# Optimization experiments

Hardware: AMD Instinct MI355X
Metric: run time of the kernel (lower is better)

The kernel has to match this reference:

```python
import jax, jax.numpy as jnp
import numpy as np

D_MODEL = 1024
NHEAD = 16
HEAD_DIM = D_MODEL // NHEAD
LN_EPS = 1e-5


def _retention_scan(v, lam_h):
    # v: (B, L, H, DH); lam_h: (H,)
    # recurrence: s_0 = v_0; s_t = lam * s_{t-1} + v_t
    B, L, H, DH = v.shape
    a = jnp.broadcast_to(lam_h[None, None, :, None], v.shape)

    def combine(x, y):
        a1, b1 = x
        a2, b2 = y
        return (a1 * a2, a2 * b1 + b2)

    _, states = jax.lax.associative_scan(combine, (a, v), axis=1)
    return states


def setup_inputs() -> dict:
    key = jax.random.key(0)
    ks = jax.random.split(key, 6)
    B, L, D = 4, 4096, D_MODEL
    s = 1.0 / np.sqrt(D)
    return {
        "x": jax.random.normal(ks[0], (B, L, D), jnp.float32),
        "Wq": jax.random.normal(ks[1], (D, D), jnp.float32) * s,
        "Wv": jax.random.normal(ks[2], (D, D), jnp.float32) * s,
        "Wg": jax.random.normal(ks[3], (D, D), jnp.float32) * s,
        "Wo": jax.random.normal(ks[4], (D, D), jnp.float32) * s,
        "beta": jnp.full((NHEAD,), -0.2, jnp.float32),
        "ln_gamma": jnp.ones((D_MODEL,), jnp.float32),
        "ln_beta": jnp.zeros((D_MODEL,), jnp.float32),
    }


def reference(x, Wq, Wv, Wg, Wo, beta, ln_gamma, ln_beta):
    B, L, D = x.shape
    H, DH = NHEAD, HEAD_DIM
    # projections (torch Linear: x @ W.T)
    q = (x @ Wq.T).reshape(B, L, H, DH)
    v = (x @ Wv.T).reshape(B, L, H, DH)
    lam_h = jax.nn.sigmoid(beta)
    state = _retention_scan(v, lam_h)  # (B, L, H, DH)
    y = (q * state).reshape(B, L, D)
    # LayerNorm over last dim
    mu = jnp.mean(y, axis=-1, keepdims=True)
    var = jnp.mean((y - mu) ** 2, axis=-1, keepdims=True)
    y = (y - mu) * jax.lax.rsqrt(var + LN_EPS) * ln_gamma + ln_beta
    # SiLU gate
    gate = jax.nn.silu(x @ Wg.T)
    y = y * gate
    return y @ Wo.T
```

## Files before the change

kernel.cpp:

```cpp
#include <hip/hip_runtime.h>

#define BB 4
#define LL 4096
#define DM 1024
#define NH 16
#define MM (BB * LL)
#define CC2 256
#define LC2 16

typedef unsigned short u16;
typedef float f32x4 __attribute__((ext_vector_type(4)));
typedef __bf16 mfma_in __attribute__((ext_vector_type(8)));

__device__ __forceinline__ u16 f2bf(float f) {
    unsigned u = __float_as_uint(f);
    u += 0x7FFFu + ((u >> 16) & 1u);
    return (u16)(u >> 16);
}
__device__ __forceinline__ float bf2f(u16 u) {
    return __uint_as_float(((unsigned)u) << 16);
}

__device__ __forceinline__ void gld_lds16(const u16* g, u16* l) {
    __builtin_amdgcn_global_load_lds(
        (const __attribute__((address_space(1))) void*)g,
        (__attribute__((address_space(3))) void*)l,
        16, 0, 0);
}

#define XF4 (MM * DM / 4)
#define WF4 (DM * DM / 4)
__global__ __launch_bounds__(256)
void cvt_all(const float* __restrict__ x,
             const float* __restrict__ w0, const float* __restrict__ w1,
             const float* __restrict__ w2, const float* __restrict__ w3,
             u16* __restrict__ dst) {
    int i = blockIdx.x * 256 + threadIdx.x;
    const float* src;
    int si;
    if (i < XF4) { src = x; si = i; }
    else {
        int j = i - XF4;
        const float* ws[4] = {w0, w1, w2, w3};
        src = ws[j >> 18];
        si = j & (WF4 - 1);
    }
    float4 f = ((const float4*)src)[si];
    ushort4 o;
    o.x = f2bf(f.x); o.y = f2bf(f.y); o.z = f2bf(f.z); o.w = f2bf(f.w);
    ((ushort4*)dst)[i] = o;
}

__device__ __forceinline__ void mainloop_bk64(
    const u16* __restrict__ A, const u16* __restrict__ B, int K,
    int mBlk, int nBlk, u16* As, u16* Bs, f32x4 acc[4][4]) {
    const int tid  = threadIdx.x;
    const int wave = tid >> 6;
    const int lane = tid & 63;
    const int quad = lane >> 4;
    const int l16  = lane & 15;
    const int wm   = (wave >> 1) * 64;
    const int wn   = (wave & 1) * 64;

    const int srow8 = wave * 8 + (lane >> 3);
    const int cOff  = ((lane & 7) ^ (lane >> 3)) * 8;

    const u16* gA[4];
    const u16* gB[4];
    u16* lA[4];
    u16* lB[4];
#pragma unroll
    for (int j = 0; j < 4; j++) {
        gA[j] = A + (size_t)(mBlk + j * 32 + srow8) * K + cOff;
        gB[j] = B + (size_t)(nBlk + j * 32 + srow8) * K + cOff;
        lA[j] = As + (j * 32 + wave * 8) * 64;
        lB[j] = Bs + (j * 32 + wave * 8) * 64;
    }

    int rowA[4], rowB[4];
#pragma unroll
    for (int i = 0; i < 4; i++) {
        rowA[i] = (wm + i * 16 + l16) * 64;
        rowB[i] = (wn + i * 16 + l16) * 64;
    }
    const int c0 = ((quad    ) ^ (l16 & 7)) * 8;
    const int c1 = ((quad + 4) ^ (l16 & 7)) * 8;

    for (int kt = 0; kt < K; kt += 64) {
        __syncthreads();
#pragma unroll
        for (int j = 0; j < 4; j++) gld_lds16(gA[j] + kt, lA[j]);
#pragma unroll
        for (int j = 0; j < 4; j++) gld_lds16(gB[j] + kt, lB[j]);
        __syncthreads();

#pragma unroll
        for (int s = 0; s < 2; s++) {
            const int cs = s ? c1 : c0;
            mfma_in af[4], bfr[4];
#pragma unroll
            for (int i = 0; i < 4; i++)
                af[i] = *(const mfma_in*)&As[rowA[i] + cs];
#pragma unroll
            for (int j = 0; j < 4; j++)
                bfr[j] = *(const mfma_in*)&Bs[rowB[j] + cs];
#pragma unroll
            for (int i = 0; i < 4; i++)
#pragma unroll
                for (int j = 0; j < 4; j++)
                    acc[i][j] = __builtin_amdgcn_mfma_f32_16x16x32_bf16(af[i], bfr[j], acc[i][j], 0, 0, 0);
        }
    }
}

__global__ __launch_bounds__(256)
void gemm_qvg(const u16* __restrict__ A, const u16* __restrict__ B,
              u16* __restrict__ oq, u16* __restrict__ ov, u16* __restrict__ og,
              int K) {
    __shared__ u16 As[128 * 64];
    __shared__ u16 Bs[128 * 64];
    const int mBlk = blockIdx.x * 128;
    const int nBlk = blockIdx.y * 128;

    f32x4 acc[4][4] = {};
    mainloop_bk64(A, B, K, mBlk, nBlk, As, Bs, acc);

    const int tid  = threadIdx.x;
    const int wave = tid >> 6;
    const int lane = tid & 63;
    const int quad = lane >> 4;
    const int l16  = lane & 15;
    const int wm   = (wave >> 1) * 64;
    const int wn   = (wave & 1) * 64;

    u16* outs[3] = {oq, ov, og};
    u16* O = outs[nBlk >> 10];
    const int nIn = nBlk & 1023;
#pragma unroll
    for (int i = 0; i < 4; i++) {
        int row0 = mBlk + wm + i * 16 + quad * 4;
#pragma unroll
        for (int j = 0; j < 4; j++) {
            int col = nIn + wn + j * 16 + l16;
#pragma unroll
            for (int r = 0; r < 4; r++)
                O[(size_t)(row0 + r) * DM + col] = f2bf(acc[i][j][r]);
        }
    }
}

__global__ __launch_bounds__(256)
void gemm_out(const u16* __restrict__ A, const u16* __restrict__ B,
              float* __restrict__ C, int N, int K) {
    __shared__ u16 As[128 * 64];
    __shared__ u16 Bs[128 * 64];
    const int mBlk = blockIdx.x * 128;
    const int nBlk = blockIdx.y * 128;

    f32x4 acc[4][4] = {};
    mainloop_bk64(A, B, K, mBlk, nBlk, As, Bs, acc);

    const int tid  = threadIdx.x;
    const int wave = tid >> 6;
    const int lane = tid & 63;
    const int quad = lane >> 4;
    const int l16  = lane & 15;
    const int wm   = (wave >> 1) * 64;
    const int wn   = (wave & 1) * 64;

#pragma unroll
    for (int i = 0; i < 4; i++) {
        int row0 = mBlk + wm + i * 16 + quad * 4;
#pragma unroll
        for (int j = 0; j < 4; j++) {
            int col = nBlk + wn + j * 16 + l16;
#pragma unroll
            for (int r = 0; r < 4; r++)
                C[(size_t)(row0 + r) * N + col] = acc[i][j][r];
        }
    }
}

__global__ __launch_bounds__(256)
void scan_ends(const u16* __restrict__ v, const float* __restrict__ beta,
               float* __restrict__ ebuf) {
    int d = blockIdx.x * 256 + threadIdx.x;
    int c = blockIdx.y, b = blockIdx.z;
    int h = d >> 6;
    float lam = 1.0f / (1.0f + __expf(-beta[h]));
    size_t idx = ((size_t)b * LL + (size_t)c * LC2) * DM + d;
    float s = 0.0f;
#pragma unroll
    for (int i = 0; i < LC2; i++) {
        s = lam * s + bf2f(v[idx]);
        idx += DM;
    }
    ebuf[((size_t)b * CC2 + c) * DM + d] = s;
}

__global__ __launch_bounds__(256)
void scan_carry(const float* __restrict__ ebuf, const float* __restrict__ beta,
                float* __restrict__ carry) {
    int ch = blockIdx.x * 256 + threadIdx.x;
    int b = ch >> 10, d = ch & 1023;
    int h = d >> 6;
    float lam = 1.0f / (1.0f + __expf(-beta[h]));
    float lamC = lam;
    for (int i = 0; i < 4; i++) lamC *= lamC;
    float cur = 0.0f;
#pragma unroll 8
    for (int c = 0; c < CC2; c++) {
        size_t idx = ((size_t)b * CC2 + c) * DM + d;
        carry[idx] = cur;
        cur = lamC * cur + ebuf[idx];
    }
}

__global__ __launch_bounds__(256)
void scan_ln_gate(const u16* __restrict__ v, const u16* __restrict__ q,
                  const u16* __restrict__ g, const float* __restrict__ carry,
                  const float* __restrict__ beta, const float* __restrict__ gamma,
                  const float* __restrict__ lnb, u16* __restrict__ out) {
    __shared__ float red[2][8];
    const int t = threadIdx.x;
    const int c = blockIdx.x, b = blockIdx.y;
    const int wave = t >> 6, lane = t & 63;
    const int d0 = t * 4;
    const int h = d0 >> 6;
    float lam = 1.0f / (1.0f + __expf(-beta[h]));
    float4 gm = ((const float4*)gamma)[t];
    float4 bt = ((const float4*)lnb)[t];
    float4 cr = *(const float4*)(carry + ((size_t)b * CC2 + c) * DM + d0);
    float s0 = cr.x, s1 = cr.y, s2 = cr.z, s3 = cr.w;
    size_t base = ((size_t)b * LL + (size_t)c * LC2) * DM + d0;

    for (int i = 0; i < LC2; i++) {
        ushort4 v4 = *(const ushort4*)(v + base);
        ushort4 q4 = *(const ushort4*)(q + base);
        ushort4 g4 = *(const ushort4*)(g + base);
        s0 = lam * s0 + bf2f(v4.x);
        s1 = lam * s1 + bf2f(v4.y);
        s2 = lam * s2 + bf2f(v4.z);
        s3 = lam * s3 + bf2f(v4.w);
        float y0 = bf2f(q4.x) * s0, y1 = bf2f(q4.y) * s1;
        float y2 = bf2f(q4.z) * s2, y3 = bf2f(q4.w) * s3;
        float sum = y0 + y1 + y2 + y3;
        float sq  = y0 * y0 + y1 * y1 + y2 * y2 + y3 * y3;
#pragma unroll
        for (int off = 32; off > 0; off >>= 1) {
            sum += __shfl_xor(sum, off);
            sq  += __shfl_xor(sq, off);
        }
        int p = i & 1;
        if (lane == 0) { red[p][wave] = sum; red[p][4 + wave] = sq; }
        __syncthreads();
        float ts = red[p][0] + red[p][1] + red[p][2] + red[p][3];
        float tq = red[p][4] + red[p][5] + red[p][6] + red[p][7];
        float mu  = ts * (1.0f / DM);
        float inv = rsqrtf(tq * (1.0f / DM) - mu * mu + 1e-5f);

        float gv0 = bf2f(g4.x), gv1 = bf2f(g4.y), gv2 = bf2f(g4.z), gv3 = bf2f(g4.w);
        float x0 = ((y0 - mu) * inv * gm.x + bt.x) * (gv0 / (1.0f + __expf(-gv0)));
        float x1 = ((y1 - mu) * inv * gm.y + bt.y) * (gv1 / (1.0f + __expf(-gv1)));
        float x2 = ((y2 - mu) * inv * gm.z + bt.z) * (gv2 / (1.0f + __expf(-gv2)));
        float x3 = ((y3 - mu) * inv * gm.w + bt.w) * (gv3 / (1.0f + __expf(-gv3)));
        ushort4 o;
        o.x = f2bf(x0); o.y = f2bf(x1); o.z = f2bf(x2); o.w = f2bf(x3);
        *(ushort4*)(out + base) = o;
        base += DM;
    }
}

extern "C" void kernel_launch(void* const* d_in, const int* in_sizes, int n_in,
                              void* d_out, int out_size, void* d_ws, size_t ws_size,
                              hipStream_t stream) {
    const float* x     = (const float*)d_in[0];
    const float* Wq    = (const float*)d_in[1];
    const float* Wv    = (const float*)d_in[2];
    const float* Wg    = (const float*)d_in[3];
    const float* Wo    = (const float*)d_in[4];
    const float* beta  = (const float*)d_in[5];
    const float* gamma = (const float*)d_in[6];
    const float* lnb   = (const float*)d_in[7];

    u16* xb  = (u16*)d_ws;
    u16* Wqb = xb + (size_t)MM * DM;
    u16* Wob = Wqb + (size_t)3 * DM * DM;
    u16* qb  = Wob + (size_t)DM * DM;
    u16* vb  = qb + (size_t)MM * DM;
    u16* gb  = vb + (size_t)MM * DM;
    float* ebuf  = (float*)(gb + (size_t)MM * DM);
    float* carry = ebuf + (size_t)BB * CC2 * DM;
    u16* yfin = xb;

    cvt_all<<<(XF4 + 4 * WF4 + 255) / 256, 256, 0, stream>>>(x, Wq, Wv, Wg, Wo, xb);

    dim3 gq(MM / 128, 3 * DM / 128);
    gemm_qvg<<<gq, 256, 0, stream>>>(xb, Wqb, qb, vb, gb, DM);

    dim3 gs(DM / 256, CC2, BB);
    scan_ends<<<gs, 256, 0, stream>>>(vb, beta, ebuf);
    scan_carry<<<(BB * DM) / 256, 256, 0, stream>>>(ebuf, beta, carry);
    dim3 gf(CC2, BB);
    scan_ln_gate<<<gf, 256, 0, stream>>>(vb, qb, gb, carry, beta, gamma, lnb, yfin);

    dim3 go(MM / 128, DM / 128);
    gemm_out<<<go, 256, 0, stream>>>(yfin, Wob, (float*)d_out, DM, DM);
}
```

Measured before the change: 346.9 us.

## Switch GEMMs to 32x32x16 MFMA and fold carry scan into LN kernel

The GEMM mainloop now uses 32x32x16 bf16 MFMA with a 2x2 tile of 16-wide accumulators per wave instead of 4x4 16x16x32 tiles. This halves the LDS fragment loads per MFMA and issues fewer, larger matrix instructions. The separate scan_carry kernel is removed: each scan_ln_gate block recomputes its carry by serially scanning all preceding chunk ends. That drops one launch and the carry buffer, but adds a serial loop of up to 255 iterations with redundant loads in later chunks.

```diff
diff --git a/kernel.cpp b/kernel.cpp
--- a/kernel.cpp
+++ b/kernel.cpp
@@ -9,7 +9,7 @@
 #define LC2 16
 
 typedef unsigned short u16;
-typedef float f32x4 __attribute__((ext_vector_type(4)));
+typedef float f32x16 __attribute__((ext_vector_type(16)));
 typedef __bf16 mfma_in __attribute__((ext_vector_type(8)));
 
 __device__ __forceinline__ u16 f2bf(float f) {
@@ -51,14 +51,14 @@
     ((ushort4*)dst)[i] = o;
 }
 
-__device__ __forceinline__ void mainloop_bk64(
+__device__ __forceinline__ void mainloop32(
     const u16* __restrict__ A, const u16* __restrict__ B, int K,
-    int mBlk, int nBlk, u16* As, u16* Bs, f32x4 acc[4][4]) {
+    int mBlk, int nBlk, u16* As, u16* Bs, f32x16 acc[2][2]) {
     const int tid  = threadIdx.x;
     const int wave = tid >> 6;
     const int lane = tid & 63;
-    const int quad = lane >> 4;
-    const int l16  = lane & 15;
+    const int l32  = lane & 31;
+    const int half = lane >> 5;
     const int wm   = (wave >> 1) * 64;
     const int wn   = (wave & 1) * 64;
 
@@ -77,14 +77,16 @@
         lB[j] = Bs + (j * 32 + wave * 8) * 64;
     }
 
-    int rowA[4], rowB[4];
-#pragma unroll
-    for (int i = 0; i < 4; i++) {
-        rowA[i] = (wm + i * 16 + l16) * 64;
-        rowB[i] = (wn + i * 16 + l16) * 64;
-    }
-    const int c0 = ((quad    ) ^ (l16 & 7)) * 8;
-    const int c1 = ((quad + 4) ^ (l16 & 7)) * 8;
+    int rowA[2], rowB[2];
+#pragma unroll
+    for (int i = 0; i < 2; i++) {
+        rowA[i] = (wm + i * 32 + l32) * 64;
+        rowB[i] = (wn + i * 32 + l32) * 64;
+    }
+    int cs[4];
+#pragma unroll
+    for (int s = 0; s < 4; s++)
+        cs[s] = ((s * 2 + half) ^ (lane & 7)) * 8;
 
     for (int kt = 0; kt < K; kt += 64) {
         __syncthreads();
@@ -95,20 +97,19 @@
         __syncthreads();
 
 #pragma unroll
-        for (int s = 0; s < 2; s++) {
-            const int cs = s ? c1 : c0;
-            mfma_in af[4], bfr[4];
-#pragma unroll
-            for (int i = 0; i < 4; i++)
-                af[i] = *(const mfma_in*)&As[rowA[i] + cs];
-#pragma unroll
-            for (int j = 0; j < 4; j++)
-                bfr[j] = *(const mfma_in*)&Bs[rowB[j] + cs];
-#pragma unroll
-            for (int i = 0; i < 4; i++)
-#pragma unroll
-                for (int j = 0; j < 4; j++)
-                    acc[i][j] = __builtin_amdgcn_mfma_f32_16x16x32_bf16(af[i], bfr[j], acc[i][j], 0, 0, 0);
+        for (int s = 0; s < 4; s++) {
+            mfma_in af[2], bfr[2];
+#pragma unroll
+            for (int i = 0; i < 2; i++)
+                af[i] = *(const mfma_in*)&As[rowA[i] + cs[s]];
+#pragma unroll
+            for (int j = 0; j < 2; j++)
+                bfr[j] = *(const mfma_in*)&Bs[rowB[j] + cs[s]];
+#pragma unroll
+            for (int i = 0; i < 2; i++)
+#pragma unroll
+                for (int j = 0; j < 2; j++)
+                    acc[i][j] = __builtin_amdgcn_mfma_f32_32x32x16_bf16(af[i], bfr[j], acc[i][j], 0, 0, 0);
         }
     }
 }
@@ -122,14 +123,14 @@
     const int mBlk = blockIdx.x * 128;
     const int nBlk = blockIdx.y * 128;
 
-    f32x4 acc[4][4] = {};
-    mainloop_bk64(A, B, K, mBlk, nBlk, As, Bs, acc);
+    f32x16 acc[2][2] = {};
+    mainloop32(A, B, K, mBlk, nBlk, As, Bs, acc);
 
     const int tid  = threadIdx.x;
     const int wave = tid >> 6;
     const int lane = tid & 63;
-    const int quad = lane >> 4;
-    const int l16  = lane & 15;
+    const int l32  = lane & 31;
+    const int half = lane >> 5;
     const int wm   = (wave >> 1) * 64;
     const int wn   = (wave & 1) * 64;
 
@@ -137,14 +138,15 @@
     u16* O = outs[nBlk >> 10];
     const int nIn = nBlk & 1023;
 #pragma unroll
-    for (int i = 0; i < 4; i++) {
-        int row0 = mBlk + wm + i * 16 + quad * 4;
-#pragma unroll
-        for (int j = 0; j < 4; j++) {
-            int col = nIn + wn + j * 16 + l16;
-#pragma unroll
-            for (int r = 0; r < 4; r++)
-                O[(size_t)(row0 + r) * DM + col] = f2bf(acc[i][j][r]);
+    for (int i = 0; i < 2; i++) {
+#pragma unroll
+        for (int j = 0; j < 2; j++) {
+            int col = nIn + wn + j * 32 + l32;
+#pragma unroll
+            for (int r = 0; r < 16; r++) {
+                int row = mBlk + wm + i * 32 + (r & 3) + 8 * (r >> 2) + 4 * half;
+                O[(size_t)row * DM + col] = f2bf(acc[i][j][r]);
+            }
         }
     }
 }
@@ -157,26 +159,27 @@
     const int mBlk = blockIdx.x * 128;
     const int nBlk = blockIdx.y * 128;
 
-    f32x4 acc[4][4] = {};
-    mainloop_bk64(A, B, K, mBlk, nBlk, As, Bs, acc);
+    f32x16 acc[2][2] = {};
+    mainloop32(A, B, K, mBlk, nBlk, As, Bs, acc);
 
     const int tid  = threadIdx.x;
     const int wave = tid >> 6;
     const int lane = tid & 63;
-    const int quad = lane >> 4;
-    const int l16  = lane & 15;
+    const int l32  = lane & 31;
+    const int half = lane >> 5;
     const int wm   = (wave >> 1) * 64;
     const int wn   = (wave & 1) * 64;
 
 #pragma unroll
-    for (int i = 0; i < 4; i++) {
-        int row0 = mBlk + wm + i * 16 + quad * 4;
-#pragma unroll
-        for (int j = 0; j < 4; j++) {
-            int col = nBlk + wn + j * 16 + l16;
-#pragma unroll
-            for (int r = 0; r < 4; r++)
-                C[(size_t)(row0 + r) * N + col] = acc[i][j][r];
+    for (int i = 0; i < 2; i++) {
+#pragma unroll
+        for (int j = 0; j < 2; j++) {
+            int col = nBlk + wn + j * 32 + l32;
+#pragma unroll
+            for (int r = 0; r < 16; r++) {
+                int row = mBlk + wm + i * 32 + (r & 3) + 8 * (r >> 2) + 4 * half;
+                C[(size_t)row * N + col] = acc[i][j][r];
+            }
         }
     }
 }
@@ -199,26 +202,8 @@
 }
 
 __global__ __launch_bounds__(256)
-void scan_carry(const float* __restrict__ ebuf, const float* __restrict__ beta,
-                float* __restrict__ carry) {
-    int ch = blockIdx.x * 256 + threadIdx.x;
-    int b = ch >> 10, d = ch & 1023;
-    int h = d >> 6;
-    float lam = 1.0f / (1.0f + __expf(-beta[h]));
-    float lamC = lam;
-    for (int i = 0; i < 4; i++) lamC *= lamC;
-    float cur = 0.0f;
-#pragma unroll 8
-    for (int c = 0; c < CC2; c++) {
-        size_t idx = ((size_t)b * CC2 + c) * DM + d;
-        carry[idx] = cur;
-        cur = lamC * cur + ebuf[idx];
-    }
-}
-
-__global__ __launch_bounds__(256)
 void scan_ln_gate(const u16* __restrict__ v, const u16* __restrict__ q,
-                  const u16* __restrict__ g, const float* __restrict__ carry,
+                  const u16* __restrict__ g, const float* __restrict__ ebuf,
                   const float* __restrict__ beta, const float* __restrict__ gamma,
                   const float* __restrict__ lnb, u16* __restrict__ out) {
     __shared__ float red[2][8];
@@ -228,10 +213,24 @@
     const int d0 = t * 4;
     const int h = d0 >> 6;
     float lam = 1.0f / (1.0f + __expf(-beta[h]));
+    float lamC = lam;
+#pragma unroll
+    for (int i = 0; i < 4; i++) lamC *= lamC;
+
+    float s0 = 0.f, s1 = 0.f, s2 = 0.f, s3 = 0.f;
+    {
+        const float4* e4 = (const float4*)(ebuf + (size_t)b * CC2 * DM + d0);
+        for (int j = 0; j < c; j++) {
+            float4 e = e4[(size_t)j * (DM / 4)];
+            s0 = lamC * s0 + e.x;
+            s1 = lamC * s1 + e.y;
+            s2 = lamC * s2 + e.z;
+            s3 = lamC * s3 + e.w;
+        }
+    }
+
     float4 gm = ((const float4*)gamma)[t];
     float4 bt = ((const float4*)lnb)[t];
-    float4 cr = *(const float4*)(carry + ((size_t)b * CC2 + c) * DM + d0);
-    float s0 = cr.x, s1 = cr.y, s2 = cr.z, s3 = cr.w;
     size_t base = ((size_t)b * LL + (size_t)c * LC2) * DM + d0;
 
     for (int i = 0; i < LC2; i++) {
@@ -289,8 +288,7 @@
     u16* qb  = Wob + (size_t)DM * DM;
     u16* vb  = qb + (size_t)MM * DM;
     u16* gb  = vb + (size_t)MM * DM;
-    float* ebuf  = (float*)(gb + (size_t)MM * DM);
-    float* carry = ebuf + (size_t)BB * CC2 * DM;
+    float* ebuf = (float*)(gb + (size_t)MM * DM);
     u16* yfin = xb;
 
     cvt_all<<<(XF4 + 4 * WF4 + 255) / 256, 256, 0, stream>>>(x, Wq, Wv, Wg, Wo, xb);
@@ -300,9 +298,8 @@
 
     dim3 gs(DM / 256, CC2, BB);
     scan_ends<<<gs, 256, 0, stream>>>(vb, beta, ebuf);
-    scan_carry<<<(BB * DM) / 256, 256, 0, stream>>>(ebuf, beta, carry);
     dim3 gf(CC2, BB);
-    scan_ln_gate<<<gf, 256, 0, stream>>>(vb, qb, gb, carry, beta, gamma, lnb, yfin);
+    scan_ln_gate<<<gf, 256, 0, stream>>>(vb, qb, gb, ebuf, beta, gamma, lnb, yfin);
 
     dim3 go(MM / 128, DM / 128);
     gemm_out<<<go, 256, 0, stream>>>(yfin, Wob, (float*)d_out, DM, DM);
```

New measurement: 388.2 us. 1.12x slower.
